# Optimization experiments

Measured on AMD Instinct MI355X. Metric: run time of the kernel, lower is better.

Reference implementation:

```python
import jax, jax.numpy as jnp
import numpy as np

N = 100000   # nodes
E = 1200000  # edges
XD = 64      # x_dim
ED = 16      # edge_attr_dim
D = 64       # hidden_size
L = 3        # n_layers
G = 512      # num graphs
C = 10       # num_class
BN_EPS = 1e-5


def setup_inputs() -> dict:
    key = jax.random.key(0)
    ks = jax.random.split(key, 30)

    def w(k, shape, scale=0.05):
        return jax.random.normal(k, shape, jnp.float32) * scale

    inp = {
        "x": jax.random.normal(ks[0], (N, XD), jnp.float32),
        "edge_index": jax.random.randint(ks[1], (2, E), 0, N),
        "batch": jnp.sort(jax.random.randint(ks[2], (N,), 0, G)),
        "edge_attr": jax.random.normal(ks[3], (E, ED), jnp.float32),
        # encoders
        "w_node": w(ks[4], (XD, D)), "b_node": jnp.zeros((D,), jnp.float32),
        "w_edge": w(ks[5], (ED, D)), "b_edge": jnp.zeros((D,), jnp.float32),
        # per-layer GINEConv params (stacked over L layers)
        "lin_w": w(ks[6], (L, D, D)), "lin_b": jnp.zeros((L, D), jnp.float32),
        "mlp1_w": w(ks[7], (L, D, D)), "mlp1_b": jnp.zeros((L, D), jnp.float32),
        "bn1_g": jnp.ones((L, D), jnp.float32), "bn1_b": jnp.zeros((L, D), jnp.float32),
        "mlp2_w": w(ks[8], (L, D, D)), "mlp2_b": jnp.zeros((L, D), jnp.float32),
        # fc_out head: MLP(D,D) -> BN -> Linear(D,C)
        "fo1_w": w(ks[9], (D, D)), "fo1_b": jnp.zeros((D,), jnp.float32),
        "fo_bn1_g": jnp.ones((D,), jnp.float32), "fo_bn1_b": jnp.zeros((D,), jnp.float32),
        "fo2_w": w(ks[10], (D, D)), "fo2_b": jnp.zeros((D,), jnp.float32),
        "fo_bn2_g": jnp.ones((D,), jnp.float32), "fo_bn2_b": jnp.zeros((D,), jnp.float32),
        "fo3_w": w(ks[11], (D, C)), "fo3_b": jnp.zeros((C,), jnp.float32),
    }
    return inp


def _bn(h, g, b):
    # training-mode BatchNorm1d: biased variance over the batch dim
    mu = h.mean(0, keepdims=True)
    var = h.var(0, keepdims=True)
    return g * (h - mu) * (var + BN_EPS) ** -0.5 + b


def reference(x, edge_index, batch, edge_attr,
              w_node, b_node, w_edge, b_edge,
              lin_w, lin_b, mlp1_w, mlp1_b, bn1_g, bn1_b, mlp2_w, mlp2_b,
              fo1_w, fo1_b, fo_bn1_g, fo_bn1_b, fo2_w, fo2_b,
              fo_bn2_g, fo_bn2_b, fo3_w, fo3_b):
    src, dst = edge_index[0], edge_index[1]  # message flows src -> dst
    h = x @ w_node + b_node                  # [N, D]
    ea0 = edge_attr @ w_edge + b_edge        # [E, D] encoded edge features
    for l in range(L):
        ea = ea0 @ lin_w[l] + lin_b[l]                      # GINEConv.lin
        m = jax.nn.relu(h[src] + ea)                        # edge messages [E, D]
        agg = jax.ops.segment_sum(m, dst, num_segments=N)   # scatter-add
        h2 = agg + h                                        # + (1 + eps) * x_r, eps = 0
        h2 = h2 @ mlp1_w[l] + mlp1_b[l]
        h2 = jax.nn.relu(_bn(h2, bn1_g[l], bn1_b[l]))
        h2 = h2 @ mlp2_w[l] + mlp2_b[l]
        h = jax.nn.relu(h2)                                 # dropout is no-op at eval
    pooled = jax.ops.segment_sum(h, batch, num_segments=G)  # global_add_pool [G, D]
    g1 = pooled @ fo1_w + fo1_b
    g1 = jax.nn.relu(_bn(g1, fo_bn1_g, fo_bn1_b))
    g1 = g1 @ fo2_w + fo2_b
    g1 = _bn(g1, fo_bn2_g, fo_bn2_b)
    return g1 @ fo3_w + fo3_b                               # logits [G, C]
```

## Files before the change

### kernel.cpp

```cpp
#include <hip/hip_runtime.h>
#include <hip/hip_fp16.h>

#define NN 100000
#define NE 1200000
#define DD 64
#define EDIM 16
#define NL 3
#define NG 512
#define NC 10
#define NB_SCAN ((NN + 255) / 256)
#define EPW 32

typedef _Float16 f16x2 __attribute__((ext_vector_type(2)));
typedef _Float16 v8h   __attribute__((ext_vector_type(8)));
typedef float    v4f   __attribute__((ext_vector_type(4)));

__device__ __forceinline__ unsigned packh2(float a, float b) {
    f16x2 v; v[0] = (_Float16)a; v[1] = (_Float16)b;
    unsigned u; __builtin_memcpy(&u, &v, 4); return u;
}
__device__ __forceinline__ float dot2f(unsigned a, unsigned b, float c) {
    f16x2 av, bv;
    __builtin_memcpy(&av, &a, 4); __builtin_memcpy(&bv, &b, 4);
#if __has_builtin(__builtin_amdgcn_fdot2)
    return __builtin_amdgcn_fdot2(av, bv, c, false);
#else
    return c + (float)av[0]*(float)bv[0] + (float)av[1]*(float)bv[1];
#endif
}

__device__ __forceinline__ void atomic_pk_add_h2(_Float16* addr, float a, float b) {
    f16x2 v; v[0] = (_Float16)a; v[1] = (_Float16)b;
#if __has_builtin(__builtin_amdgcn_global_atomic_fadd_v2f16)
    typedef __attribute__((address_space(1))) f16x2 gh2;
    __builtin_amdgcn_global_atomic_fadd_v2f16((gh2*)addr, v);
#else
    unsigned* u = (unsigned*)addr;
    unsigned old = *u, assumed;
    do {
        assumed = old;
        f16x2 w; __builtin_memcpy(&w, &assumed, 4);
        w = w + v;
        unsigned nv; __builtin_memcpy(&nv, &w, 4);
        old = atomicCAS(u, assumed, nv);
    } while (old != assumed);
#endif
}

__device__ __forceinline__ void bn_sc_sh(float s, float q, float g, float b,
                                         float invc, float& sc, float& sh) {
    float mu  = s * invc;
    float var = fmaxf(q * invc - mu * mu, 0.f);
    float x = var + 1e-5f;
    float r = rsqrtf(x);
    r = r * (1.5f - 0.5f * x * r * r);
    sc = g * r;
    sh = b - mu * sc;
}

__global__ __launch_bounds__(1024) void prep_kernel(
    const float* __restrict__ w_edge, const float* __restrict__ b_edge,
    const float* __restrict__ lin_w, const float* __restrict__ lin_b,
    unsigned* __restrict__ Wc16, float* __restrict__ bc)
{
    __shared__ float sWc[1024];
    const int l = blockIdx.x;
    const int tid = threadIdx.x;
    const float* Lw = lin_w + l * 4096;
    const int k = tid >> 6, col = tid & 63;
    float acc = 0.f;
    for (int j = 0; j < 64; ++j) acc = fmaf(w_edge[k*64 + j], Lw[j*64 + col], acc);
    sWc[k*64 + col] = acc;
    if (tid < 64) {
        float a = lin_b[l*64 + tid];
        for (int j = 0; j < 64; ++j) a = fmaf(b_edge[j], Lw[j*64 + tid], a);
        bc[l*64 + tid] = a;
    }
    __syncthreads();
    if (tid < 512) {
        const int j = tid >> 6, c = tid & 63;
        Wc16[l*512 + j*64 + c] = packh2(sWc[(2*j)*64 + c], sWc[(2*j+1)*64 + c]);
    }
}

__global__ __launch_bounds__(512) void pack_w_kernel(
    const float* __restrict__ w_node, const float* __restrict__ mlp1_w,
    const float* __restrict__ mlp2_w, v8h* __restrict__ Wpk)
{
    const int m = blockIdx.x;
    const float* W = (m == 0) ? w_node
                   : (m <= 3) ? mlp1_w + (m-1)*4096
                              : mlp2_w + (m-4)*4096;
    const int fid = threadIdx.x >> 6;
    const int l   = threadIdx.x & 63;
    const int t = fid >> 1, f = fid & 1;
    const int n  = (l & 15) + 16*t;
    const int kb = f*32 + (l >> 4)*8;
    v8h v;
    #pragma unroll
    for (int j = 0; j < 8; ++j) v[j] = (_Float16)W[(kb + j)*64 + n];
    Wpk[m*512 + fid*64 + l] = v;
}

__global__ __launch_bounds__(256) void hist_kernel(
    const int* __restrict__ dst, int* __restrict__ counts)
{
    const int e = blockIdx.x * 256 + threadIdx.x;
    if (e < NE) atomicAdd(&counts[dst[e]], 1);
}

__global__ __launch_bounds__(256) void scan_reduce_kernel(
    const int* __restrict__ counts, int* __restrict__ bsum)
{
    __shared__ int sd[256];
    const int t = threadIdx.x;
    const int idx = blockIdx.x * 256 + t;
    sd[t] = (idx < NN) ? counts[idx] : 0;
    __syncthreads();
    for (int off = 128; off > 0; off >>= 1) {
        if (t < off) sd[t] += sd[t + off];
        __syncthreads();
    }
    if (t == 0) bsum[blockIdx.x] = sd[0];
}

__global__ __launch_bounds__(512) void scan_partials_kernel(
    const int* __restrict__ bsum, int* __restrict__ bscan)
{
    __shared__ int sd[512];
    const int t = threadIdx.x;
    sd[t] = (t < NB_SCAN) ? bsum[t] : 0;
    __syncthreads();
    for (int off = 1; off < 512; off <<= 1) {
        int u = (t >= off) ? sd[t - off] : 0;
        __syncthreads();
        sd[t] += u;
        __syncthreads();
    }
    if (t < NB_SCAN) bscan[t] = (t == 0) ? 0 : sd[t - 1];
}

__global__ __launch_bounds__(256) void scan_final_kernel(
    const int* __restrict__ counts, const int* __restrict__ bscan,
    int* __restrict__ rowptr, int* __restrict__ next)
{
    __shared__ int sd[256];
    const int t = threadIdx.x;
    const int idx = blockIdx.x * 256 + t;
    const int v = (idx < NN) ? counts[idx] : 0;
    sd[t] = v;
    __syncthreads();
    for (int off = 1; off < 256; off <<= 1) {
        int u = (t >= off) ? sd[t - off] : 0;
        __syncthreads();
        sd[t] += u;
        __syncthreads();
    }
    const int excl = sd[t] - v + bscan[blockIdx.x];
    if (idx < NN) { rowptr[idx] = excl; next[idx] = excl; }
    if (idx == NN - 1) rowptr[NN] = excl + v;
}

__global__ __launch_bounds__(256) void scatter_kernel(
    const int* __restrict__ src, const int* __restrict__ dst,
    const float* __restrict__ edge_attr,
    int* __restrict__ next, int* __restrict__ csr_src, uint4* __restrict__ csr_ea)
{
    const int e = blockIdx.x * 256 + threadIdx.x;
    if (e >= NE) return;
    const float4* q = (const float4*)(edge_attr + (size_t)e * 16);
    float4 a0 = q[0], a1 = q[1], a2 = q[2], a3 = q[3];
    const int pos = atomicAdd(&next[dst[e]], 1);
    csr_src[pos] = src[e];
    uint4 A, B;
    A.x = packh2(a0.x, a0.y); A.y = packh2(a0.z, a0.w);
    A.z = packh2(a1.x, a1.y); A.w = packh2(a1.z, a1.w);
    B.x = packh2(a2.x, a2.y); B.y = packh2(a2.z, a2.w);
    B.z = packh2(a3.x, a3.y); B.w = packh2(a3.z, a3.w);
    csr_ea[(size_t)pos*2 + 0] = A;
    csr_ea[(size_t)pos*2 + 1] = B;
}

__global__ __launch_bounds__(256) void agg_edge_kernel(
    const int* __restrict__ rowptr, const int* __restrict__ csr_src,
    const uint4* __restrict__ csr_ea,
    const unsigned* __restrict__ Wc16, const float* __restrict__ bc,
    const _Float16* __restrict__ h16, _Float16* __restrict__ agg16)
{
    __shared__ uint4 sEA[4][64];
    __shared__ int   sSRC[4][32];
    const int tid  = threadIdx.x;
    const int lane = tid & 63;
    const int wv   = tid >> 6;
    const int wid  = blockIdx.x * 4 + wv;
    const int e0   = wid * EPW;

    sEA[wv][lane] = csr_ea[(size_t)e0 * 2 + lane];
    if (lane < 32) sSRC[wv][lane] = csr_src[e0 + lane];

    unsigned wq[8];
    #pragma unroll
    for (int j = 0; j < 8; ++j) wq[j] = Wc16[j*64 + lane];
    const float mb = bc[lane];

    int lo = 0;
    {
        int idx = lane * 1563; if (idx > NN) idx = NN;
        lo += (__popcll(__ballot(rowptr[idx] <= e0)) - 1) * 1563;
        idx = lo + lane * 25; if (idx > NN) idx = NN;
        lo += (__popcll(__ballot(rowptr[idx] <= e0)) - 1) * 25;
        idx = lo + lane; if (idx > NN) idx = NN;
        lo += __popcll(__ballot(rowptr[idx] <= e0)) - 1;
    }
    int cur = lo;
    int nb  = rowptr[cur + 1];
    float acc = 0.f;

    __syncthreads();

    const uint4* eaw = sEA[wv];
    const int*   srw = sSRC[wv];

    auto msg = [&](uint4 A, uint4 B, float hv) -> float {
        float m = mb;
        m = dot2f(A.x, wq[0], m); m = dot2f(A.y, wq[1], m);
        m = dot2f(A.z, wq[2], m); m = dot2f(A.w, wq[3], m);
        m = dot2f(B.x, wq[4], m); m = dot2f(B.y, wq[5], m);
        m = dot2f(B.z, wq[6], m); m = dot2f(B.w, wq[7], m);
        return fmaxf(m + hv, 0.f);
    };
    auto flush = [&](int node, float v) {
        float other = __shfl_xor(v, 1);
        if ((lane & 1) == 0)
            atomic_pk_add_h2(agg16 + (size_t)node*64 + lane, v, other);
    };
    auto adv = [&](int q) {
        flush(cur, acc); acc = 0.f;
        do { ++cur; } while (rowptr[cur + 1] <= q);
        nb = rowptr[cur + 1];
    };
    auto doGroup = [&](int g, float hv0, float hv1, float hv2, float hv3) {
        const int p = e0 + g*4;
        float m0, m1, m2, m3;
        { uint4 A = eaw[g*8+0], B = eaw[g*8+1]; m0 = msg(A, B, hv0); }
        { uint4 A = eaw[g*8+2], B = eaw[g*8+3]; m1 = msg(A, B, hv1); }
        { uint4 A = eaw[g*8+4], B = eaw[g*8+5]; m2 = msg(A, B, hv2); }
        { uint4 A = eaw[g*8+6], B = eaw[g*8+7]; m3 = msg(A, B, hv3); }
        if (p + 3 < nb) {
            acc += (m0 + m1) + (m2 + m3);
        } else {
            if (p     >= nb) adv(p);     acc += m0;
            if (p + 1 >= nb) adv(p + 1); acc += m1;
            if (p + 2 >= nb) adv(p + 2); acc += m2;
            if (p + 3 >= nb) adv(p + 3); acc += m3;
        }
    };

    _Float16 a0, a1, a2, a3, b0, b1, b2, b3;
    {
        const int4 s = *(const int4*)&srw[0];
        a0 = h16[(size_t)s.x*64 + lane]; a1 = h16[(size_t)s.y*64 + lane];
        a2 = h16[(size_t)s.z*64 + lane]; a3 = h16[(size_t)s.w*64 + lane];
    }
    #pragma unroll 1
    for (int gp = 0; gp < EPW/8; ++gp) {
        const int g0 = gp*2, g1 = g0 + 1;
        {
            const int4 s = *(const int4*)&srw[g1*4];
            b0 = h16[(size_t)s.x*64 + lane]; b1 = h16[(size_t)s.y*64 + lane];
            b2 = h16[(size_t)s.z*64 + lane]; b3 = h16[(size_t)s.w*64 + lane];
        }
        doGroup(g0, (float)a0, (float)a1, (float)a2, (float)a3);
        if (gp + 1 < EPW/8) {
            const int4 s = *(const int4*)&srw[(g1 + 1)*4];
            a0 = h16[(size_t)s.x*64 + lane]; a1 = h16[(size_t)s.y*64 + lane];
            a2 = h16[(size_t)s.z*64 + lane]; a3 = h16[(size_t)s.w*64 + lane];
        }
        doGroup(g1, (float)b0, (float)b1, (float)b2, (float)b3);
    }
    flush(cur, acc);
}

template<bool IN_HALF, bool ADD_B, bool TRANS, bool OUT_RELU, bool OUT_ACCUM,
         bool OUT_F32, bool OUT_HALF, bool OUT_POOL>
__global__ __launch_bounds__(256) void mfma_gemm_kernel(
    const float* __restrict__ in0, const _Float16* __restrict__ in16,
    const _Float16* __restrict__ in16b,
    const v8h* __restrict__ Wpk, const float* __restrict__ bias,
    const float* __restrict__ bni_sum, const float* __restrict__ bni_sumsq,
    const float* __restrict__ bni_g, const float* __restrict__ bni_b,
    float bni_invc,
    float* __restrict__ out, _Float16* __restrict__ out16,
    float* __restrict__ bn_sum, float* __restrict__ bn_sumsq,
    const int* __restrict__ batch, float* __restrict__ pooled)
{
    __shared__ float sS[1024];
    __shared__ float sQ[1024];
    __shared__ float sSc[64], sSh[64];
    const int tid = threadIdx.x;
    const int wv = tid >> 6, l = tid & 63;
    const int li = l & 15, quad = l >> 4;
    const int rb = (blockIdx.x * 4 + wv) * 16;
    const bool active = (rb < NN);

    if constexpr (TRANS) {
        if (tid < 64)
            bn_sc_sh(bni_sum[tid], bni_sumsq[tid], bni_g[tid], bni_b[tid],
                     bni_invc, sSc[tid], sSh[tid]);
        __syncthreads();
    }

    v8h Bf[8];
    #pragma unroll
    for (int i = 0; i < 8; ++i) Bf[i] = Wpk[i*64 + l];

    v4f acc[4] = {v4f{0,0,0,0}, v4f{0,0,0,0}, v4f{0,0,0,0}, v4f{0,0,0,0}};

    if (active) {
        v8h Af[2];
        if constexpr (IN_HALF) {
            const size_t off = (size_t)(rb + li)*64 + quad*8;
            Af[0] = *(const v8h*)(in16 + off);
            Af[1] = *(const v8h*)(in16 + off + 32);
            if constexpr (ADD_B) {
                Af[0] += *(const v8h*)(in16b + off);
                Af[1] += *(const v8h*)(in16b + off + 32);
            }
        } else {
            const float* arow = in0 + (size_t)(rb + li)*64 + quad*8;
            #pragma unroll
            for (int f = 0; f < 2; ++f) {
                float4 x0 = *(const float4*)(arow + f*32);
                float4 x1 = *(const float4*)(arow + f*32 + 4);
                if constexpr (TRANS) {
                    const int kb = f*32 + quad*8;
                    float4 s0 = *(const float4*)(sSc + kb);
                    float4 s1 = *(const float4*)(sSc + kb + 4);
                    float4 t0 = *(const float4*)(sSh + kb);
                    float4 t1 = *(const float4*)(sSh + kb + 4);
                    x0.x = fmaxf(fmaf(x0.x, s0.x, t0.x), 0.f);
                    x0.y = fmaxf(fmaf(x0.y, s0.y, t0.y), 0.f);
                    x0.z = fmaxf(fmaf(x0.z, s0.z, t0.z), 0.f);
                    x0.w = fmaxf(fmaf(x0.w, s0.w, t0.w), 0.f);
                    x1.x = fmaxf(fmaf(x1.x, s1.x, t1.x), 0.f);
                    x1.y = fmaxf(fmaf(x1.y, s1.y, t1.y), 0.f);
                    x1.z = fmaxf(fmaf(x1.z, s1.z, t1.z), 0.f);
                    x1.w = fmaxf(fmaf(x1.w, s1.w, t1.w), 0.f);
                }
                v8h a;
                a[0] = (_Float16)x0.x; a[1] = (_Float16)x0.y;
                a[2] = (_Float16)x0.z; a[3] = (_Float16)x0.w;
                a[4] = (_Float16)x1.x; a[5] = (_Float16)x1.y;
                a[6] = (_Float16)x1.z; a[7] = (_Float16)x1.w;
                Af[f] = a;
            }
        }
        #pragma unroll
        for (int t = 0; t < 4; ++t) {
            acc[t] = __builtin_amdgcn_mfma_f32_16x16x32_f16(Af[0], Bf[t*2+0], acc[t], 0, 0, 0);
            acc[t] = __builtin_amdgcn_mfma_f32_16x16x32_f16(Af[1], Bf[t*2+1], acc[t], 0, 0, 0);
        }
    }

    if constexpr (OUT_F32 || OUT_HALF || OUT_ACCUM) {
        float ps[4] = {0.f, 0.f, 0.f, 0.f}, pq[4] = {0.f, 0.f, 0.f, 0.f};
        if (active) {
            #pragma unroll
            for (int t = 0; t < 4; ++t) {
                const int col = li + 16*t;
                const float bcol = bias[col];
                #pragma unroll
                for (int r = 0; r < 4; ++r) {
                    const int row = rb + quad*4 + r;
                    float v = acc[t][r] + bcol;
                    if constexpr (OUT_ACCUM) { ps[t] += v; pq[t] += v*v; }
                    if constexpr (OUT_RELU) v = fmaxf(v, 0.f);
                    if constexpr (OUT_F32)  out[(size_t)row*64 + col] = v;
                    if constexpr (OUT_HALF) out16[(size_t)row*64 + col] = (_Float16)v;
                }
            }
        }
        if constexpr (OUT_ACCUM) {
            #pragma unroll
            for (int t = 0; t < 4; ++t) {
                sS[wv*256 + l*4 + t] = ps[t];
                sQ[wv*256 + l*4 + t] = pq[t];
            }
            __syncthreads();
            if (tid < 64) {
                const int t = tid >> 4, li2 = tid & 15;
                float s = 0.f, q = 0.f;
                #pragma unroll
                for (int w = 0; w < 4; ++w)
                    #pragma unroll
                    for (int qd = 0; qd < 4; ++qd) {
                        const int idx = w*256 + (qd*16 + li2)*4 + t;
                        s += sS[idx]; q += sQ[idx];
                    }
                atomicAdd(bn_sum + tid, s);
                atomicAdd(bn_sumsq + tid, q);
            }
        }
    }

    if constexpr (OUT_POOL) {
        if (active) {
            const int b0  = batch[rb];
            const int b15 = batch[rb + 15];
            if (b0 == b15) {
                #pragma unroll
                for (int t = 0; t < 4; ++t) {
                    const int col = li + 16*t;
                    const float bcol = bias[col];
                    float s = 0.f;
                    #pragma unroll
                    for (int r = 0; r < 4; ++r)
                        s += fmaxf(acc[t][r] + bcol, 0.f);
                    s += __shfl_xor(s, 16);
                    s += __shfl_xor(s, 32);
                    if (quad == 0) atomicAdd(&pooled[b0*64 + col], s);
                }
            } else {
                #pragma unroll
                for (int t = 0; t < 4; ++t) {
                    const int col = li + 16*t;
                    const float bcol = bias[col];
                    #pragma unroll
                    for (int r = 0; r < 4; ++r) {
                        const int row = rb + quad*4 + r;
                        const float v = fmaxf(acc[t][r] + bcol, 0.f);
                        atomicAdd(&pooled[batch[row]*64 + col], v);
                    }
                }
            }
        }
    }
}

template<int IN_MODE, bool OUT_RELU, bool OUT_ACCUM>
__global__ __launch_bounds__(256) void gemm64_kernel(
    const float* __restrict__ in0,
    const float* __restrict__ W, const float* __restrict__ bias,
    const float* __restrict__ bni_sum, const float* __restrict__ bni_sumsq,
    const float* __restrict__ bni_g, const float* __restrict__ bni_b,
    float bni_invc,
    float* __restrict__ out, int nrows,
    float* __restrict__ bn_sum, float* __restrict__ bn_sumsq)
{
    __shared__ __align__(16) float sIn[64*64];
    __shared__ float sRedS[512];
    __shared__ float sRedQ[512];
    __shared__ __align__(16) float sSc[64], sSh[64];
    const int tid = threadIdx.x;
    const int c  = tid & 31;
    const int rg = tid >> 5;
    const int r0 = blockIdx.x * 64;

    if constexpr (IN_MODE == 2) {
        if (tid < 64)
            bn_sc_sh(bni_sum[tid], bni_sumsq[tid], bni_g[tid], bni_b[tid],
                     bni_invc, sSc[tid], sSh[tid]);
        __syncthreads();
    }

    float w0[64], w1[64];
    #pragma unroll
    for (int k = 0; k < 64; ++k) { w0[k] = W[k*64 + c]; w1[k] = W[k*64 + c + 32]; }
    const float b0 = bias[c], b1 = bias[c + 32];

    for (int i = tid; i < 1024; i += 256) {
        const int r  = i >> 4;
        const int c4 = (i & 15) * 4;
        const int gr = r0 + r;
        float4 v = make_float4(0.f, 0.f, 0.f, 0.f);
        if (gr < nrows) {
            v = *(const float4*)(in0 + (size_t)gr*64 + c4);
            if constexpr (IN_MODE == 2) {
                float4 s4 = *(const float4*)(sSc + c4);
                float4 h4 = *(const float4*)(sSh + c4);
                v.x = fmaxf(fmaf(v.x, s4.x, h4.x), 0.f);
                v.y = fmaxf(fmaf(v.y, s4.y, h4.y), 0.f);
                v.z = fmaxf(fmaf(v.z, s4.z, h4.z), 0.f);
                v.w = fmaxf(fmaf(v.w, s4.w, h4.w), 0.f);
            }
        }
        *(float4*)(sIn + r*64 + c4) = v;
    }
    __syncthreads();

    float ps0 = 0.f, psq0 = 0.f, ps1 = 0.f, psq1 = 0.f;
    #pragma unroll
    for (int i = 0; i < 8; ++i) {
        const int r = rg + 8*i;
        float a0 = b0, a1 = b1;
        #pragma unroll
        for (int k = 0; k < 64; k += 4) {
            float4 a = *(const float4*)(sIn + r*64 + k);
            a0 = fmaf(a.x, w0[k+0], a0); a1 = fmaf(a.x, w1[k+0], a1);
            a0 = fmaf(a.y, w0[k+1], a0); a1 = fmaf(a.y, w1[k+1], a1);
            a0 = fmaf(a.z, w0[k+2], a0); a1 = fmaf(a.z, w1[k+2], a1);
            a0 = fmaf(a.w, w0[k+3], a0); a1 = fmaf(a.w, w1[k+3], a1);
        }
        const int gr = r0 + r;
        if (gr < nrows) {
            if constexpr (OUT_ACCUM) {
                ps0 += a0; psq0 += a0*a0;
                ps1 += a1; psq1 += a1*a1;
            }
            out[(size_t)gr*64 + c]      = OUT_RELU ? fmaxf(a0, 0.f) : a0;
            out[(size_t)gr*64 + c + 32] = OUT_RELU ? fmaxf(a1, 0.f) : a1;
        }
    }

    if constexpr (OUT_ACCUM) {
        sRedS[rg*64 + c]      = ps0;
        sRedS[rg*64 + c + 32] = ps1;
        sRedQ[rg*64 + c]      = psq0;
        sRedQ[rg*64 + c + 32] = psq1;
        __syncthreads();
        if (tid < 64) {
            float s = 0.f, q = 0.f;
            #pragma unroll
            for (int g = 0; g < 8; ++g) { s += sRedS[g*64 + tid]; q += sRedQ[g*64 + tid]; }
            atomicAdd(bn_sum + tid, s);
            atomicAdd(bn_sumsq + tid, q);
        }
    }
}

__global__ __launch_bounds__(256) void head_final_kernel(
    const float* __restrict__ hb,
    const float* __restrict__ bni_sum, const float* __restrict__ bni_sumsq,
    const float* __restrict__ bni_g, const float* __restrict__ bni_b,
    float bni_invc,
    const float* __restrict__ fo3_w, const float* __restrict__ fo3_b,
    float* __restrict__ out)
{
    __shared__ float sSc[64], sSh[64];
    const int tid = threadIdx.x;
    if (tid < 64)
        bn_sc_sh(bni_sum[tid], bni_sumsq[tid], bni_g[tid], bni_b[tid],
                 bni_invc, sSc[tid], sSh[tid]);
    __syncthreads();
    const int idx = blockIdx.x * 256 + tid;
    if (idx >= NG * NC) return;
    const int g = idx / NC, c = idx % NC;
    float acc = fo3_b[c];
    for (int k = 0; k < 64; ++k) {
        float v = fmaf(hb[g*64 + k], sSc[k], sSh[k]);
        acc = fmaf(v, fo3_w[k*NC + c], acc);
    }
    out[idx] = acc;
}

extern "C" void kernel_launch(void* const* d_in, const int* in_sizes, int n_in,
                              void* d_out, int out_size, void* d_ws, size_t ws_size,
                              hipStream_t stream) {
    const float* x         = (const float*)d_in[0];
    const int*   edge_index= (const int*)  d_in[1];
    const int*   batch     = (const int*)  d_in[2];
    const float* edge_attr = (const float*)d_in[3];
    const float* w_node    = (const float*)d_in[4];
    const float* b_node    = (const float*)d_in[5];
    const float* w_edge    = (const float*)d_in[6];
    const float* b_edge    = (const float*)d_in[7];
    const float* lin_w     = (const float*)d_in[8];
    const float* lin_b     = (const float*)d_in[9];
    const float* mlp1_w    = (const float*)d_in[10];
    const float* mlp1_b    = (const float*)d_in[11];
    const float* bn1_g     = (const float*)d_in[12];
    const float* bn1_b     = (const float*)d_in[13];
    const float* mlp2_w    = (const float*)d_in[14];
    const float* mlp2_b    = (const float*)d_in[15];
    const float* fo1_w     = (const float*)d_in[16];
    const float* fo1_b     = (const float*)d_in[17];
    const float* fo_bn1_g  = (const float*)d_in[18];
    const float* fo_bn1_b  = (const float*)d_in[19];
    const float* fo2_w     = (const float*)d_in[20];
    const float* fo2_b     = (const float*)d_in[21];
    const float* fo_bn2_g  = (const float*)d_in[22];
    const float* fo_bn2_b  = (const float*)d_in[23];
    const float* fo3_w     = (const float*)d_in[24];
    const float* fo3_b     = (const float*)d_in[25];
    float* out = (float*)d_out;

    char* ws = (char*)d_ws;
    float* t    = (float*)(ws);
    int* counts = (int*)t;
    int* next   = (int*)t + NN;
    int*   csr_src = (int*)(ws + 25600000);
    uint4* csr_ea  = (uint4*)(ws + 30400000);
    int* rowptr = (int*)(ws + 68800000);
    _Float16* h16   = (_Float16*)(ws + 69300000);
    _Float16* agg16 = (_Float16*)(ws + 82100000);
    float* sm   = (float*)(ws + 94900000);
    unsigned* Wc16 = (unsigned*)sm;
    float* bc       = sm + 1536;
    float* bnbuf    = sm + 1728;
    float* pooled   = sm + 2368;
    float* ha       = sm + 35136;
    float* hb       = sm + 67904;
    int* bsum       = (int*)(sm + 100672);
    int* bscan      = bsum + 512;
    v8h* Wpk        = (v8h*)(sm + 101696);

    const int* src = edge_index;
    const int* dst = edge_index + NE;

    const int mfma_blocks  = (NN/16 + 3) / 4;
    const int edge_blocks  = (NE + 255) / 256;
    const int aggE_blocks  = NE / (EPW * 4);

    prep_kernel<<<NL, 1024, 0, stream>>>(w_edge, b_edge, lin_w, lin_b, Wc16, bc);
    pack_w_kernel<<<7, 512, 0, stream>>>(w_node, mlp1_w, mlp2_w, Wpk);

    mfma_gemm_kernel<false, false, false, false, false, false, true, false>
        <<<mfma_blocks, 256, 0, stream>>>(
        x, nullptr, nullptr, Wpk, b_node,
        nullptr, nullptr, nullptr, nullptr, 0.f,
        nullptr, h16, nullptr, nullptr, nullptr, nullptr);

    hipMemsetAsync(counts, 0, NN * sizeof(int), stream);
    hipMemsetAsync(bnbuf, 0, (640 + 32768) * sizeof(float), stream);
    hist_kernel<<<edge_blocks, 256, 0, stream>>>(dst, counts);
    scan_reduce_kernel<<<NB_SCAN, 256, 0, stream>>>(counts, bsum);
    scan_partials_kernel<<<1, 512, 0, stream>>>(bsum, bscan);
    scan_final_kernel<<<NB_SCAN, 256, 0, stream>>>(counts, bscan, rowptr, next);
    scatter_kernel<<<edge_blocks, 256, 0, stream>>>(
        src, dst, edge_attr, next, csr_src, csr_ea);

    for (int l = 0; l < NL; ++l) {
        float* bnL = bnbuf + l * 128;
        hipMemsetAsync(agg16, 0, (size_t)NN * DD * sizeof(_Float16), stream);
        agg_edge_kernel<<<aggE_blocks, 256, 0, stream>>>(
            rowptr, csr_src, csr_ea, Wc16 + l*512, bc + l*64, h16, agg16);
        mfma_gemm_kernel<true, true, false, false, true, true, false, false>
            <<<mfma_blocks, 256, 0, stream>>>(
            nullptr, agg16, h16, Wpk + (1+l)*512, mlp1_b + l*64,
            nullptr, nullptr, nullptr, nullptr, 0.f,
            t, nullptr, bnL, bnL + 64, nullptr, nullptr);
        if (l < NL - 1) {
            mfma_gemm_kernel<false, false, true, true, false, false, true, false>
                <<<mfma_blocks, 256, 0, stream>>>(
                t, nullptr, nullptr, Wpk + (4+l)*512, mlp2_b + l*64,
                bnL, bnL + 64, bn1_g + l*64, bn1_b + l*64, 1.0f / NN,
                nullptr, h16, nullptr, nullptr, nullptr, nullptr);
        } else {
            mfma_gemm_kernel<false, false, true, true, false, false, false, true>
                <<<mfma_blocks, 256, 0, stream>>>(
                t, nullptr, nullptr, Wpk + (4+l)*512, mlp2_b + l*64,
                bnL, bnL + 64, bn1_g + l*64, bn1_b + l*64, 1.0f / NN,
                nullptr, nullptr, nullptr, nullptr, batch, pooled);
        }
    }

    float* bnH1 = bnbuf + 3 * 128;
    float* bnH2 = bnbuf + 4 * 128;
    gemm64_kernel<0, false, true><<<NG/64, 256, 0, stream>>>(
        pooled, fo1_w, fo1_b,
        nullptr, nullptr, nullptr, nullptr, 0.f,
        ha, NG, bnH1, bnH1 + 64);
    gemm64_kernel<2, false, true><<<NG/64, 256, 0, stream>>>(
        ha, fo2_w, fo2_b,
        bnH1, bnH1 + 64, fo_bn1_g, fo_bn1_b, 1.0f / NG,
        hb, NG, bnH2, bnH2 + 64);
    head_final_kernel<<<(NG*NC + 255)/256, 256, 0, stream>>>(
        hb, bnH2, bnH2 + 64, fo_bn2_g, fo_bn2_b, 1.0f / NG,
        fo3_w, fo3_b, out);
}
```

Before: 716.9 us.

## Fuse CSR aggregation with MLP1 GEMM per node block, drop atomics and agg buffer

Replaces the edge-balanced aggregation kernel, which used packed fp16 global atomics into a zeroed agg buffer, with a node-blocked kernel. Each wave aggregates the incoming edges of 16 destination nodes into an LDS tile, adds h, and immediately runs the MLP1 MFMA, also accumulating BN statistics. This removes the per-layer agg memset, the atomics and the agg round trip through memory. The MLP1 output is now stored in fp16 instead of fp32, which halves that traffic but costs precision. Work per wave now follows node degree rather than a fixed edge count, so load imbalance across waves is possible.

```diff
diff --git a/kernel.cpp b/kernel.cpp
--- a/kernel.cpp
+++ b/kernel.cpp
@@ -9,7 +9,7 @@
 #define NG 512
 #define NC 10
 #define NB_SCAN ((NN + 255) / 256)
-#define EPW 32
+#define NBLK ((NN + 63) / 64)
 
 typedef _Float16 f16x2 __attribute__((ext_vector_type(2)));
 typedef _Float16 v8h   __attribute__((ext_vector_type(8)));
@@ -26,24 +26,6 @@
     return __builtin_amdgcn_fdot2(av, bv, c, false);
 #else
     return c + (float)av[0]*(float)bv[0] + (float)av[1]*(float)bv[1];
-#endif
-}
-
-__device__ __forceinline__ void atomic_pk_add_h2(_Float16* addr, float a, float b) {
-    f16x2 v; v[0] = (_Float16)a; v[1] = (_Float16)b;
-#if __has_builtin(__builtin_amdgcn_global_atomic_fadd_v2f16)
-    typedef __attribute__((address_space(1))) f16x2 gh2;
-    __builtin_amdgcn_global_atomic_fadd_v2f16((gh2*)addr, v);
-#else
-    unsigned* u = (unsigned*)addr;
-    unsigned old = *u, assumed;
-    do {
-        assumed = old;
-        f16x2 w; __builtin_memcpy(&w, &assumed, 4);
-        w = w + v;
-        unsigned nv; __builtin_memcpy(&nv, &w, 4);
-        old = atomicCAS(u, assumed, nv);
-    } while (old != assumed);
 #endif
 }
 
@@ -181,45 +163,51 @@
     csr_ea[(size_t)pos*2 + 1] = B;
 }
 
-__global__ __launch_bounds__(256) void agg_edge_kernel(
-    const int* __restrict__ rowptr, const int* __restrict__ csr_src,
-    const uint4* __restrict__ csr_ea,
+__global__ __launch_bounds__(256) void agg_mlp1_kernel(
+    const int* __restrict__ rowptr,
+    const int* __restrict__ csr_src, const uint4* __restrict__ csr_ea,
     const unsigned* __restrict__ Wc16, const float* __restrict__ bc,
-    const _Float16* __restrict__ h16, _Float16* __restrict__ agg16)
-{
-    __shared__ uint4 sEA[4][64];
-    __shared__ int   sSRC[4][32];
+    const _Float16* __restrict__ h16,
+    const v8h* __restrict__ Wpk, const float* __restrict__ bias,
+    _Float16* __restrict__ t16,
+    float* __restrict__ bn_sum, float* __restrict__ bn_sumsq)
+{
+    __shared__ int rp[65];
+    __shared__ __align__(16) _Float16 tile[4][16*72];
+    __shared__ __align__(16) char uni[4][2048];
+    __shared__ __align__(16) int sSRC[4][64];
+
     const int tid  = threadIdx.x;
     const int lane = tid & 63;
     const int wv   = tid >> 6;
-    const int wid  = blockIdx.x * 4 + wv;
-    const int e0   = wid * EPW;
-
-    sEA[wv][lane] = csr_ea[(size_t)e0 * 2 + lane];
-    if (lane < 32) sSRC[wv][lane] = csr_src[e0 + lane];
+    const int n0   = blockIdx.x * 64;
+
+    if (tid < 65) {
+        int idx = n0 + tid; if (idx > NN) idx = NN;
+        rp[tid] = rowptr[idx];
+    }
+    {
+        unsigned* tz = (unsigned*)tile[wv];
+        #pragma unroll
+        for (int i = 0; i < 9; ++i) tz[lane + i*64] = 0u;
+    }
 
     unsigned wq[8];
     #pragma unroll
     for (int j = 0; j < 8; ++j) wq[j] = Wc16[j*64 + lane];
     const float mb = bc[lane];
 
-    int lo = 0;
-    {
-        int idx = lane * 1563; if (idx > NN) idx = NN;
-        lo += (__popcll(__ballot(rowptr[idx] <= e0)) - 1) * 1563;
-        idx = lo + lane * 25; if (idx > NN) idx = NN;
-        lo += (__popcll(__ballot(rowptr[idx] <= e0)) - 1) * 25;
-        idx = lo + lane; if (idx > NN) idx = NN;
-        lo += __popcll(__ballot(rowptr[idx] <= e0)) - 1;
-    }
-    int cur = lo;
-    int nb  = rowptr[cur + 1];
+    __syncthreads();
+
+    const int nwb  = 16 * wv;
+    const int e0   = rp[nwb];
+    const int eEnd = rp[nwb + 16];
+    int cur = nwb;
+    int nb  = rp[cur + 1];
     float acc = 0.f;
 
-    __syncthreads();
-
-    const uint4* eaw = sEA[wv];
-    const int*   srw = sSRC[wv];
+    uint4*     sEAw  = (uint4*)uni[wv];
+    _Float16*  tileW = tile[wv];
 
     auto msg = [&](uint4 A, uint4 B, float hv) -> float {
         float m = mb;
@@ -229,23 +217,19 @@
         m = dot2f(B.z, wq[6], m); m = dot2f(B.w, wq[7], m);
         return fmaxf(m + hv, 0.f);
     };
-    auto flush = [&](int node, float v) {
-        float other = __shfl_xor(v, 1);
-        if ((lane & 1) == 0)
-            atomic_pk_add_h2(agg16 + (size_t)node*64 + lane, v, other);
+    auto adv = [&](int q) {
+        tileW[(cur - nwb)*72 + lane] = (_Float16)acc;
+        acc = 0.f;
+        do { ++cur; } while (rp[cur + 1] <= q);
+        nb = rp[cur + 1];
     };
-    auto adv = [&](int q) {
-        flush(cur, acc); acc = 0.f;
-        do { ++cur; } while (rowptr[cur + 1] <= q);
-        nb = rowptr[cur + 1];
-    };
-    auto doGroup = [&](int g, float hv0, float hv1, float hv2, float hv3) {
-        const int p = e0 + g*4;
+    auto doGroup = [&](const uint4* eg, int p,
+                       float hv0, float hv1, float hv2, float hv3) {
         float m0, m1, m2, m3;
-        { uint4 A = eaw[g*8+0], B = eaw[g*8+1]; m0 = msg(A, B, hv0); }
-        { uint4 A = eaw[g*8+2], B = eaw[g*8+3]; m1 = msg(A, B, hv1); }
-        { uint4 A = eaw[g*8+4], B = eaw[g*8+5]; m2 = msg(A, B, hv2); }
-        { uint4 A = eaw[g*8+6], B = eaw[g*8+7]; m3 = msg(A, B, hv3); }
+        { uint4 A = eg[0], B = eg[1]; m0 = msg(A, B, hv0); }
+        { uint4 A = eg[2], B = eg[3]; m1 = msg(A, B, hv1); }
+        { uint4 A = eg[4], B = eg[5]; m2 = msg(A, B, hv2); }
+        { uint4 A = eg[6], B = eg[7]; m3 = msg(A, B, hv3); }
         if (p + 3 < nb) {
             acc += (m0 + m1) + (m2 + m3);
         } else {
@@ -256,46 +240,120 @@
         }
     };
 
-    _Float16 a0, a1, a2, a3, b0, b1, b2, b3;
-    {
-        const int4 s = *(const int4*)&srw[0];
-        a0 = h16[(size_t)s.x*64 + lane]; a1 = h16[(size_t)s.y*64 + lane];
-        a2 = h16[(size_t)s.z*64 + lane]; a3 = h16[(size_t)s.w*64 + lane];
-    }
-    #pragma unroll 1
-    for (int gp = 0; gp < EPW/8; ++gp) {
-        const int g0 = gp*2, g1 = g0 + 1;
-        {
-            const int4 s = *(const int4*)&srw[g1*4];
-            b0 = h16[(size_t)s.x*64 + lane]; b1 = h16[(size_t)s.y*64 + lane];
-            b2 = h16[(size_t)s.z*64 + lane]; b3 = h16[(size_t)s.w*64 + lane];
-        }
-        doGroup(g0, (float)a0, (float)a1, (float)a2, (float)a3);
-        if (gp + 1 < EPW/8) {
-            const int4 s = *(const int4*)&srw[(g1 + 1)*4];
-            a0 = h16[(size_t)s.x*64 + lane]; a1 = h16[(size_t)s.y*64 + lane];
-            a2 = h16[(size_t)s.z*64 + lane]; a3 = h16[(size_t)s.w*64 + lane];
-        }
-        doGroup(g1, (float)b0, (float)b1, (float)b2, (float)b3);
-    }
-    flush(cur, acc);
-}
-
-template<bool IN_HALF, bool ADD_B, bool TRANS, bool OUT_RELU, bool OUT_ACCUM,
-         bool OUT_F32, bool OUT_HALF, bool OUT_POOL>
+    for (int base = e0; base < eEnd; base += 64) {
+        const int cnt = min(64, eEnd - base);
+        if (lane < 2*cnt)      sEAw[lane]      = csr_ea[(size_t)base*2 + lane];
+        if (64 + lane < 2*cnt) sEAw[64 + lane] = csr_ea[(size_t)base*2 + 64 + lane];
+        if (lane < cnt)        sSRC[wv][lane]  = csr_src[base + lane];
+
+        const int grpN = cnt >> 2;
+        if (grpN) {
+            int4 s = *(const int4*)&sSRC[wv][0];
+            _Float16 hA0 = h16[(size_t)s.x*64 + lane];
+            _Float16 hA1 = h16[(size_t)s.y*64 + lane];
+            _Float16 hA2 = h16[(size_t)s.z*64 + lane];
+            _Float16 hA3 = h16[(size_t)s.w*64 + lane];
+            #pragma unroll 1
+            for (int gp = 0; gp < grpN; ++gp) {
+                const int gn = (gp + 1 < grpN) ? gp + 1 : gp;
+                int4 sn = *(const int4*)&sSRC[wv][gn*4];
+                _Float16 hB0 = h16[(size_t)sn.x*64 + lane];
+                _Float16 hB1 = h16[(size_t)sn.y*64 + lane];
+                _Float16 hB2 = h16[(size_t)sn.z*64 + lane];
+                _Float16 hB3 = h16[(size_t)sn.w*64 + lane];
+                doGroup(sEAw + gp*8, base + gp*4,
+                        (float)hA0, (float)hA1, (float)hA2, (float)hA3);
+                hA0 = hB0; hA1 = hB1; hA2 = hB2; hA3 = hB3;
+            }
+        }
+        for (int k = grpN*4; k < cnt; ++k) {
+            const int p = base + k;
+            const int sv = sSRC[wv][k];
+            const float hv = (float)h16[(size_t)sv*64 + lane];
+            uint4 A = sEAw[k*2], B = sEAw[k*2 + 1];
+            const float m = msg(A, B, hv);
+            if (p >= nb) adv(p);
+            acc += m;
+        }
+    }
+    if (e0 < eEnd)
+        tileW[(cur - nwb)*72 + lane] = (_Float16)acc;
+
+    const int l2 = lane;
+    const int li = l2 & 15, quad = l2 >> 4;
+    const int rb = n0 + nwb;
+    const bool active = (rb < NN);
+
+    v8h Bf[8];
+    #pragma unroll
+    for (int i = 0; i < 8; ++i) Bf[i] = Wpk[i*64 + l2];
+
+    v4f accm[4] = {v4f{0,0,0,0}, v4f{0,0,0,0}, v4f{0,0,0,0}, v4f{0,0,0,0}};
+    if (active) {
+        const _Float16* trow = tileW + li*72 + quad*8;
+        v8h Af0 = *(const v8h*)(trow);
+        v8h Af1 = *(const v8h*)(trow + 32);
+        const size_t off = (size_t)(rb + li)*64 + quad*8;
+        Af0 += *(const v8h*)(h16 + off);
+        Af1 += *(const v8h*)(h16 + off + 32);
+        #pragma unroll
+        for (int t = 0; t < 4; ++t) {
+            accm[t] = __builtin_amdgcn_mfma_f32_16x16x32_f16(Af0, Bf[t*2+0], accm[t], 0, 0, 0);
+            accm[t] = __builtin_amdgcn_mfma_f32_16x16x32_f16(Af1, Bf[t*2+1], accm[t], 0, 0, 0);
+        }
+    }
+
+    float ps[4] = {0.f, 0.f, 0.f, 0.f}, pq[4] = {0.f, 0.f, 0.f, 0.f};
+    if (active) {
+        #pragma unroll
+        for (int t = 0; t < 4; ++t) {
+            const int col = li + 16*t;
+            const float bcol = bias[col];
+            #pragma unroll
+            for (int r = 0; r < 4; ++r) {
+                const int row = rb + quad*4 + r;
+                float v = accm[t][r] + bcol;
+                ps[t] += v; pq[t] += v*v;
+                t16[(size_t)row*64 + col] = (_Float16)v;
+            }
+        }
+    }
+
+    float* sSw = (float*)uni[wv];
+    float* sQw = sSw + 256;
+    #pragma unroll
+    for (int t = 0; t < 4; ++t) {
+        sSw[l2*4 + t] = ps[t];
+        sQw[l2*4 + t] = pq[t];
+    }
+    __syncthreads();
+    if (tid < 64) {
+        const int t = tid >> 4, li2 = tid & 15;
+        float s = 0.f, q = 0.f;
+        #pragma unroll
+        for (int w = 0; w < 4; ++w) {
+            const float* pS = (const float*)uni[w];
+            #pragma unroll
+            for (int qd = 0; qd < 4; ++qd) {
+                const int idx = (qd*16 + li2)*4 + t;
+                s += pS[idx]; q += pS[256 + idx];
+            }
+        }
+        atomicAdd(bn_sum + tid, s);
+        atomicAdd(bn_sumsq + tid, q);
+    }
+}
+
+template<int IN_MODE, bool OUT_RELU, bool OUT_HALF, bool OUT_POOL>
 __global__ __launch_bounds__(256) void mfma_gemm_kernel(
     const float* __restrict__ in0, const _Float16* __restrict__ in16,
-    const _Float16* __restrict__ in16b,
     const v8h* __restrict__ Wpk, const float* __restrict__ bias,
     const float* __restrict__ bni_sum, const float* __restrict__ bni_sumsq,
     const float* __restrict__ bni_g, const float* __restrict__ bni_b,
     float bni_invc,
-    float* __restrict__ out, _Float16* __restrict__ out16,
-    float* __restrict__ bn_sum, float* __restrict__ bn_sumsq,
+    _Float16* __restrict__ out16,
     const int* __restrict__ batch, float* __restrict__ pooled)
 {
-    __shared__ float sS[1024];
-    __shared__ float sQ[1024];
     __shared__ float sSc[64], sSh[64];
     const int tid = threadIdx.x;
     const int wv = tid >> 6, l = tid & 63;
@@ -303,7 +361,7 @@
     const int rb = (blockIdx.x * 4 + wv) * 16;
     const bool active = (rb < NN);
 
-    if constexpr (TRANS) {
+    if constexpr (IN_MODE == 2) {
         if (tid < 64)
             bn_sc_sh(bni_sum[tid], bni_sumsq[tid], bni_g[tid], bni_b[tid],
                      bni_invc, sSc[tid], sSh[tid]);
@@ -318,35 +376,25 @@
 
     if (active) {
         v8h Af[2];
-        if constexpr (IN_HALF) {
-            const size_t off = (size_t)(rb + li)*64 + quad*8;
-            Af[0] = *(const v8h*)(in16 + off);
-            Af[1] = *(const v8h*)(in16 + off + 32);
-            if constexpr (ADD_B) {
-                Af[0] += *(const v8h*)(in16b + off);
-                Af[1] += *(const v8h*)(in16b + off + 32);
-            }
+        if constexpr (IN_MODE == 2) {
+            const _Float16* arow = in16 + (size_t)(rb + li)*64 + quad*8;
+            v8h r0 = *(const v8h*)(arow);
+            v8h r1 = *(const v8h*)(arow + 32);
+            v8h a0, a1;
+            #pragma unroll
+            for (int j = 0; j < 8; ++j) {
+                const int k0 = quad*8 + j;
+                const int k1 = 32 + quad*8 + j;
+                a0[j] = (_Float16)fmaxf(fmaf((float)r0[j], sSc[k0], sSh[k0]), 0.f);
+                a1[j] = (_Float16)fmaxf(fmaf((float)r1[j], sSc[k1], sSh[k1]), 0.f);
+            }
+            Af[0] = a0; Af[1] = a1;
         } else {
             const float* arow = in0 + (size_t)(rb + li)*64 + quad*8;
             #pragma unroll
             for (int f = 0; f < 2; ++f) {
                 float4 x0 = *(const float4*)(arow + f*32);
                 float4 x1 = *(const float4*)(arow + f*32 + 4);
-                if constexpr (TRANS) {
-                    const int kb = f*32 + quad*8;
-                    float4 s0 = *(const float4*)(sSc + kb);
-                    float4 s1 = *(const float4*)(sSc + kb + 4);
-                    float4 t0 = *(const float4*)(sSh + kb);
-                    float4 t1 = *(const float4*)(sSh + kb + 4);
-                    x0.x = fmaxf(fmaf(x0.x, s0.x, t0.x), 0.f);
-                    x0.y = fmaxf(fmaf(x0.y, s0.y, t0.y), 0.f);
-                    x0.z = fmaxf(fmaf(x0.z, s0.z, t0.z), 0.f);
-                    x0.w = fmaxf(fmaf(x0.w, s0.w, t0.w), 0.f);
-                    x1.x = fmaxf(fmaf(x1.x, s1.x, t1.x), 0.f);
-                    x1.y = fmaxf(fmaf(x1.y, s1.y, t1.y), 0.f);
-                    x1.z = fmaxf(fmaf(x1.z, s1.z, t1.z), 0.f);
-                    x1.w = fmaxf(fmaf(x1.w, s1.w, t1.w), 0.f);
-                }
                 v8h a;
                 a[0] = (_Float16)x0.x; a[1] = (_Float16)x0.y;
                 a[2] = (_Float16)x0.z; a[3] = (_Float16)x0.w;
@@ -362,8 +410,7 @@
         }
     }
 
-    if constexpr (OUT_F32 || OUT_HALF || OUT_ACCUM) {
-        float ps[4] = {0.f, 0.f, 0.f, 0.f}, pq[4] = {0.f, 0.f, 0.f, 0.f};
+    if constexpr (OUT_HALF) {
         if (active) {
             #pragma unroll
             for (int t = 0; t < 4; ++t) {
@@ -373,32 +420,9 @@
                 for (int r = 0; r < 4; ++r) {
                     const int row = rb + quad*4 + r;
                     float v = acc[t][r] + bcol;
-                    if constexpr (OUT_ACCUM) { ps[t] += v; pq[t] += v*v; }
                     if constexpr (OUT_RELU) v = fmaxf(v, 0.f);
-                    if constexpr (OUT_F32)  out[(size_t)row*64 + col] = v;
-                    if constexpr (OUT_HALF) out16[(size_t)row*64 + col] = (_Float16)v;
+                    out16[(size_t)row*64 + col] = (_Float16)v;
                 }
-            }
-        }
-        if constexpr (OUT_ACCUM) {
-            #pragma unroll
-            for (int t = 0; t < 4; ++t) {
-                sS[wv*256 + l*4 + t] = ps[t];
-                sQ[wv*256 + l*4 + t] = pq[t];
-            }
-            __syncthreads();
-            if (tid < 64) {
-                const int t = tid >> 4, li2 = tid & 15;
-                float s = 0.f, q = 0.f;
-                #pragma unroll
-                for (int w = 0; w < 4; ++w)
-                    #pragma unroll
-                    for (int qd = 0; qd < 4; ++qd) {
-                        const int idx = w*256 + (qd*16 + li2)*4 + t;
-                        s += sS[idx]; q += sQ[idx];
-                    }
-                atomicAdd(bn_sum + tid, s);
-                atomicAdd(bn_sumsq + tid, q);
             }
         }
     }
@@ -585,14 +609,13 @@
     float* out = (float*)d_out;
 
     char* ws = (char*)d_ws;
-    float* t    = (float*)(ws);
-    int* counts = (int*)t;
-    int* next   = (int*)t + NN;
+    _Float16* t16 = (_Float16*)(ws);
+    int* counts = (int*)ws;
+    int* next   = (int*)ws + NN;
     int*   csr_src = (int*)(ws + 25600000);
     uint4* csr_ea  = (uint4*)(ws + 30400000);
     int* rowptr = (int*)(ws + 68800000);
     _Float16* h16   = (_Float16*)(ws + 69300000);
-    _Float16* agg16 = (_Float16*)(ws + 82100000);
     float* sm   = (float*)(ws + 94900000);
     unsigned* Wc16 = (unsigned*)sm;
     float* bc       = sm + 1536;
@@ -609,16 +632,14 @@
 
     const int mfma_blocks  = (NN/16 + 3) / 4;
     const int edge_blocks  = (NE + 255) / 256;
-    const int aggE_blocks  = NE / (EPW * 4);
 
     prep_kernel<<<NL, 1024, 0, stream>>>(w_edge, b_edge, lin_w, lin_b, Wc16, bc);
     pack_w_kernel<<<7, 512, 0, stream>>>(w_node, mlp1_w, mlp2_w, Wpk);
 
-    mfma_gemm_kernel<false, false, false, false, false, false, true, false>
-        <<<mfma_blocks, 256, 0, stream>>>(
-        x, nullptr, nullptr, Wpk, b_node,
+    mfma_gemm_kernel<0, false, true, false><<<mfma_blocks, 256, 0, stream>>>(
+        x, nullptr, Wpk, b_node,
         nullptr, nullptr, nullptr, nullptr, 0.f,
-        nullptr, h16, nullptr, nullptr, nullptr, nullptr);
+        h16, nullptr, nullptr);
 
     hipMemsetAsync(counts, 0, NN * sizeof(int), stream);
     hipMemsetAsync(bnbuf, 0, (640 + 32768) * sizeof(float), stream);
@@ -631,26 +652,19 @@
 
     for (int l = 0; l < NL; ++l) {
         float* bnL = bnbuf + l * 128;
-        hipMemsetAsync(agg16, 0, (size_t)NN * DD * sizeof(_Float16), stream);
-        agg_edge_kernel<<<aggE_blocks, 256, 0, stream>>>(
-            rowptr, csr_src, csr_ea, Wc16 + l*512, bc + l*64, h16, agg16);
-        mfma_gemm_kernel<true, true, false, false, true, true, false, false>
-            <<<mfma_blocks, 256, 0, stream>>>(
-            nullptr, agg16, h16, Wpk + (1+l)*512, mlp1_b + l*64,
-            nullptr, nullptr, nullptr, nullptr, 0.f,
-            t, nullptr, bnL, bnL + 64, nullptr, nullptr);
+        agg_mlp1_kernel<<<NBLK, 256, 0, stream>>>(
+            rowptr, csr_src, csr_ea, Wc16 + l*512, bc + l*64, h16,
+            Wpk + (1+l)*512, mlp1_b + l*64, t16, bnL, bnL + 64);
         if (l < NL - 1) {
-            mfma_gemm_kernel<false, false, true, true, false, false, true, false>
-                <<<mfma_blocks, 256, 0, stream>>>(
-                t, nullptr, nullptr, Wpk + (4+l)*512, mlp2_b + l*64,
+            mfma_gemm_kernel<2, true, true, false><<<mfma_blocks, 256, 0, stream>>>(
+                nullptr, t16, Wpk + (4+l)*512, mlp2_b + l*64,
                 bnL, bnL + 64, bn1_g + l*64, bn1_b + l*64, 1.0f / NN,
-                nullptr, h16, nullptr, nullptr, nullptr, nullptr);
+                h16, nullptr, nullptr);
         } else {
-            mfma_gemm_kernel<false, false, true, true, false, false, false, true>
-                <<<mfma_blocks, 256, 0, stream>>>(
-                t, nullptr, nullptr, Wpk + (4+l)*512, mlp2_b + l*64,
+            mfma_gemm_kernel<2, false, false, true><<<mfma_blocks, 256, 0, stream>>>(
+                nullptr, t16, Wpk + (4+l)*512, mlp2_b + l*64,
                 bnL, bnL + 64, bn1_g + l*64, bn1_b + l*64, 1.0f / NN,
-                nullptr, nullptr, nullptr, nullptr, batch, pooled);
+                nullptr, batch, pooled);
         }
     }
 
```

After: 655.5 us. 1.09x faster.
